# Optimization experiments

Hardware: AMD Instinct MI355X
Metric: run time of the kernel (lower is better)

## Reference

```python
import jax, jax.numpy as jnp
import numpy as np

NS = 16   # scalar multiplicity (ns)
NV = 4    # vector multiplicity (nv)
N_EDGE_FEAT = 3 * NS          # 48
W_NUMEL = NS * NS + NS * NV   # 320 = fully-connected TP weight numel


def setup_inputs() -> dict:
    key = jax.random.key(0)
    ks = jax.random.split(key, 8)
    N, E = 50000, 600000
    node_attr = jax.random.normal(ks[0], (N, NS), jnp.float32)          # 16x0e node features
    edge_index = jax.random.randint(ks[1], (2, E), 0, N)                # [src; dst]
    edge_attr = jax.random.normal(ks[2], (E, NS), jnp.float32)          # embedded edge attr (ns)
    edge_sh = jax.random.normal(ks[3], (E, 9), jnp.float32)             # sh lmax=2: 1+3+5
    s = 0.05
    fc1_w = jax.random.normal(ks[4], (N_EDGE_FEAT, N_EDGE_FEAT), jnp.float32) * s
    fc1_b = jnp.zeros((N_EDGE_FEAT,), jnp.float32)
    fc2_w = jax.random.normal(ks[5], (N_EDGE_FEAT, W_NUMEL), jnp.float32) * s
    fc2_b = jnp.zeros((W_NUMEL,), jnp.float32)
    return {"node_attr": node_attr, "edge_attr": edge_attr, "edge_sh": edge_sh,
            "fc1_w": fc1_w, "fc1_b": fc1_b, "fc2_w": fc2_w, "fc2_b": fc2_b,
            "edge_index": edge_index}


def reference(node_attr, edge_attr, edge_sh, fc1_w, fc1_b, fc2_w, fc2_b, edge_index):
    """TensorProductConvLayer forward: gather -> per-edge weighted tensor product -> scatter-mean.
    in_irreps=16x0e, sh=1x0e+1x1o+1x2e, out_irreps=16x0e+4x1o (residual=False, batch_norm=False)."""
    src, dst = edge_index[0], edge_index[1]
    E = edge_attr.shape[0]
    N = node_attr.shape[0]
    # edge feature = cat(edge_attr, scalar node feats of src and dst)  -> [E, 48]
    ea = jnp.concatenate([edge_attr, node_attr[src], node_attr[dst]], axis=-1)
    # fc MLP -> per-edge tensor-product weights [E, 320]
    h = jax.nn.relu(ea @ fc1_w + fc1_b)
    w = h @ fc2_w + fc2_b
    w0 = w[:, : NS * NS].reshape(E, NS, NS)   # path 0e x 0e -> 0e
    w1 = w[:, NS * NS :].reshape(E, NS, NV)   # path 0e x 1o -> 1o
    x = node_attr[dst]                        # gathered scalar features [E, 16]
    inv = 1.0 / jnp.sqrt(jnp.float32(NS))     # e3nn path normalization (fan-in = 16)
    sh0 = edge_sh[:, :1]                      # l=0 component
    sh1 = edge_sh[:, 1:4]                     # l=1 components
    out0 = jnp.einsum('eu,euw->ew', x * sh0, w0) * inv           # [E, 16]
    out1 = jnp.einsum('eu,em,euw->ewm', x, sh1, w1) * inv        # [E, 4, 3]
    msg = jnp.concatenate([out0, out1.reshape(E, NV * 3)], axis=-1)  # [E, 28]
    # scatter-mean to source nodes
    summed = jax.ops.segment_sum(msg, src, num_segments=N)
    cnt = jax.ops.segment_sum(jnp.ones((E, 1), msg.dtype), src, num_segments=N)
    return summed / jnp.maximum(cnt, 1.0)
```

## Files before the change

### kernel.cpp

```cpp
#include <hip/hip_runtime.h>

#define NS   16
#define NV   4
#define FEAT 48
#define WN   320
#define MSG  28
#define MSGB 32

typedef __bf16 bf16x8 __attribute__((ext_vector_type(8)));
typedef __bf16 bf16x4 __attribute__((ext_vector_type(4)));
typedef float  f32x4  __attribute__((ext_vector_type(4)));

#define PK1_ELEMS (2 * 3 * 64 * 8)
#define PK2_ELEMS (2 * 20 * 64 * 8)
#define PACK_BLOCKS 8

__global__ void prep_kernel(const float* __restrict__ fc1_w, const float* __restrict__ fc1_b,
                            const float* __restrict__ fc2_w, const float* __restrict__ fc2_b,
                            const int* __restrict__ src,
                            __bf16* __restrict__ pk1, __bf16* __restrict__ pk2,
                            int* __restrict__ count, int* __restrict__ pos, int E)
{
    const int tid = threadIdx.x;
    if (blockIdx.x < PACK_BLOCKS) {
        const int idx = blockIdx.x * 256 + tid;
        const int stride = PACK_BLOCKS * 256;
        for (int i = idx; i < PK1_ELEMS; i += stride) {
            const int j = i & 7, l = (i >> 3) & 63, f = i >> 9;
            const int nt = f % 3, p = f / 3;
            const int q = l >> 4, col = 16 * nt + (l & 15);
            float v;
            if (p == 0) {
                const int k = (j < 4) ? (4 * q + j) : (16 + 4 * q + j - 4);
                v = fc1_w[k * FEAT + col];
            } else if (j < 4) {
                v = fc1_w[(32 + 4 * q + j) * FEAT + col];
            } else {
                v = (j == 4 && q == 0) ? fc1_b[col] : 0.f;
            }
            pk1[i] = (__bf16)v;
        }
        for (int i = idx; i < PK2_ELEMS; i += stride) {
            const int j = i & 7, l = (i >> 3) & 63, f = i >> 9;
            const int nt = f % 20, p = f / 20;
            const int q = l >> 4, col = 16 * nt + (l & 15);
            float v;
            if (p == 0) {
                const int k = (j < 4) ? (4 * q + j) : (16 + 4 * q + j - 4);
                v = fc2_w[k * WN + col];
            } else if (j < 4) {
                v = fc2_w[(32 + 4 * q + j) * WN + col];
            } else {
                v = (j == 4 && q == 0) ? fc2_b[col] : 0.f;
            }
            pk2[i] = (__bf16)v;
        }
    } else {
        const int nb = gridDim.x - PACK_BLOCKS;
        for (int e = (blockIdx.x - PACK_BLOCKS) * 256 + tid; e < E; e += nb * 256)
            pos[e] = atomicAdd(&count[src[e]], 1);
    }
}

__global__ void scan_atomic(const int* __restrict__ in, int* __restrict__ outBase,
                            int* __restrict__ gctr, int n)
{
    __shared__ int s[256];
    __shared__ int blockBase;
    const int tid = threadIdx.x;
    const int i = blockIdx.x * 256 + tid;
    int v = (i < n) ? in[i] : 0;
    int acc = v;
    s[tid] = acc;
    __syncthreads();
    #pragma unroll
    for (int off = 1; off < 256; off <<= 1) {
        int t = (tid >= off) ? s[tid - off] : 0;
        __syncthreads();
        acc += t;
        s[tid] = acc;
        __syncthreads();
    }
    if (tid == 255) blockBase = atomicAdd(gctr, acc);
    __syncthreads();
    if (i < n) outBase[i] = blockBase + acc - v;
}

template<int MODE>
__global__ __launch_bounds__(256, 7) void edge_mfma_kernel(
    const float* __restrict__ node_attr,
    const float* __restrict__ edge_attr,
    const float* __restrict__ edge_sh,
    const int*   __restrict__ edge_index,
    const int*   __restrict__ base,
    const int*   __restrict__ pos,
    const __bf16* __restrict__ pk1,
    const __bf16* __restrict__ pk2,
    __bf16* __restrict__ msg,
    float*  __restrict__ out_acc,
    float*  __restrict__ cnt,
    int E)
{
    __shared__ float sX[4][32][20];

    const int tid = threadIdx.x;
    const int w   = tid >> 6;
    const int l   = tid & 63;
    const int q   = l >> 4;
    const int r16 = l & 15;
    const int e0  = (blockIdx.x * 4 + w) * 32;

    const float4 z4 = make_float4(0.f, 0.f, 0.f, 0.f);
    const float bias1 = (q == 0) ? 1.f : 0.f;

    bf16x8 w1f[2][3];
    #pragma unroll
    for (int p = 0; p < 2; ++p)
        #pragma unroll
        for (int nt = 0; nt < 3; ++nt)
            w1f[p][nt] = *reinterpret_cast<const bf16x8*>(pk1 + ((size_t)(p * 3 + nt) * 64 + l) * 8);

    bf16x8 eaf[2][2];
    int   srcI[2], rnkQ[2];
    bool  evt[2];
    float sh0[2], sh1[2];
    #pragma unroll
    for (int t = 0; t < 2; ++t) {
        const int e = e0 + 16 * t + r16;
        const bool ev = (e < E);
        evt[t] = ev;
        srcI[t] = ev ? edge_index[e] : 0;
        const int dstI = ev ? edge_index[E + e] : 0;

        rnkQ[t] = 0;
        if (MODE == 0 && q == 0 && ev)
            rnkQ[t] = base[srcI[t]] + pos[e];

        float4 ea4 = z4, sa4 = z4, da4 = z4;
        if (ev) {
            ea4 = *reinterpret_cast<const float4*>(edge_attr + (size_t)e * NS + 4 * q);
            sa4 = *reinterpret_cast<const float4*>(node_attr + (size_t)srcI[t] * NS + 4 * q);
            da4 = *reinterpret_cast<const float4*>(node_attr + (size_t)dstI * NS + 4 * q);
        }
        *reinterpret_cast<f32x4*>(&sX[w][16 * t + r16][4 * q]) =
            f32x4{da4.x, da4.y, da4.z, da4.w};

        bf16x8 f0, f1;
        f0[0]=(__bf16)ea4.x; f0[1]=(__bf16)ea4.y; f0[2]=(__bf16)ea4.z; f0[3]=(__bf16)ea4.w;
        f0[4]=(__bf16)sa4.x; f0[5]=(__bf16)sa4.y; f0[6]=(__bf16)sa4.z; f0[7]=(__bf16)sa4.w;
        f1[0]=(__bf16)da4.x; f1[1]=(__bf16)da4.y; f1[2]=(__bf16)da4.z; f1[3]=(__bf16)da4.w;
        f1[4]=(__bf16)bias1; f1[5]=(__bf16)0.f; f1[6]=(__bf16)0.f; f1[7]=(__bf16)0.f;
        eaf[t][0] = f0;
        eaf[t][1] = f1;
        sh0[t] = ev ? edge_sh[(size_t)e * 9] : 0.f;
        sh1[t] = (ev && q < 3) ? edge_sh[(size_t)e * 9 + 1 + q] : 0.f;
    }

    bf16x8 hc[2][2];
    #pragma unroll
    for (int t = 0; t < 2; ++t) {
        f32x4 h0 = {0.f,0.f,0.f,0.f}, h1 = {0.f,0.f,0.f,0.f}, h2 = {0.f,0.f,0.f,0.f};
        h0 = __builtin_amdgcn_mfma_f32_16x16x32_bf16(w1f[0][0], eaf[t][0], h0, 0, 0, 0);
        h0 = __builtin_amdgcn_mfma_f32_16x16x32_bf16(w1f[1][0], eaf[t][1], h0, 0, 0, 0);
        h1 = __builtin_amdgcn_mfma_f32_16x16x32_bf16(w1f[0][1], eaf[t][0], h1, 0, 0, 0);
        h1 = __builtin_amdgcn_mfma_f32_16x16x32_bf16(w1f[1][1], eaf[t][1], h1, 0, 0, 0);
        h2 = __builtin_amdgcn_mfma_f32_16x16x32_bf16(w1f[0][2], eaf[t][0], h2, 0, 0, 0);
        h2 = __builtin_amdgcn_mfma_f32_16x16x32_bf16(w1f[1][2], eaf[t][1], h2, 0, 0, 0);
        bf16x8 c0, c1;
        #pragma unroll
        for (int g = 0; g < 4; ++g) {
            c0[g]     = (__bf16)fmaxf(h0[g], 0.f);
            c0[4 + g] = (__bf16)fmaxf(h1[g], 0.f);
            c1[g]     = (__bf16)fmaxf(h2[g], 0.f);
        }
        c1[4] = (__bf16)bias1;
        c1[5] = (__bf16)0.f; c1[6] = (__bf16)0.f; c1[7] = (__bf16)0.f;
        hc[t][0] = c0;
        hc[t][1] = c1;
    }

    f32x4 acc0[2] = {{0.f,0.f,0.f,0.f},{0.f,0.f,0.f,0.f}};
    f32x4 acc1[2] = {{0.f,0.f,0.f,0.f},{0.f,0.f,0.f,0.f}};
    #pragma unroll 4
    for (int nt2 = 0; nt2 < 20; ++nt2) {
        const bf16x8 wf0 = *reinterpret_cast<const bf16x8*>(pk2 + ((size_t)(0 * 20 + nt2) * 64 + l) * 8);
        const bf16x8 wf1 = *reinterpret_cast<const bf16x8*>(pk2 + ((size_t)(1 * 20 + nt2) * 64 + l) * 8);
        #pragma unroll
        for (int t = 0; t < 2; ++t) {
            f32x4 d = {0.f,0.f,0.f,0.f};
            d = __builtin_amdgcn_mfma_f32_16x16x32_bf16(wf0, hc[t][0], d, 0, 0, 0);
            d = __builtin_amdgcn_mfma_f32_16x16x32_bf16(wf1, hc[t][1], d, 0, 0, 0);
            if (nt2 < 16) {
                const float xv = sX[w][16 * t + r16][nt2];
                #pragma unroll
                for (int g = 0; g < 4; ++g) acc0[t][g] = fmaf(xv, d[g], acc0[t][g]);
            } else {
                const float xu = sX[w][16 * t + r16][4 * (nt2 - 16) + q];
                #pragma unroll
                for (int g = 0; g < 4; ++g) acc1[t][g] = fmaf(xu, d[g], acc1[t][g]);
            }
        }
    }

    const float inv = 0.25f;

    #pragma unroll
    for (int t = 0; t < 2; ++t)
        #pragma unroll
        for (int g = 0; g < 4; ++g) {
            float s = acc1[t][g];
            s += __shfl_xor(s, 16);
            s += __shfl_xor(s, 32);
            acc1[t][g] = s;
        }

    #pragma unroll
    for (int t = 0; t < 2; ++t) {
        const int e = e0 + 16 * t + r16;
        if (e >= E) continue;
        if (MODE == 0) {
            const int rnk = __shfl(rnkQ[t], r16);
            const size_t mb = (size_t)rnk * MSGB;
            bf16x4 v4;
            #pragma unroll
            for (int g = 0; g < 4; ++g) v4[g] = (__bf16)(inv * sh0[t] * acc0[t][g]);
            *reinterpret_cast<bf16x4*>(msg + mb + 4 * q) = v4;
            if (q < 3) {
                #pragma unroll
                for (int g = 0; g < 4; ++g)
                    msg[mb + 16 + 3 * g + q] =
                        (__bf16)(inv * sh1[t] * acc1[t][g]);
            }
        } else {
            const size_t ob = (size_t)srcI[t] * MSG;
            #pragma unroll
            for (int g = 0; g < 4; ++g)
                atomicAdd(&out_acc[ob + 4 * q + g], inv * sh0[t] * acc0[t][g]);
            if (q < 3) {
                #pragma unroll
                for (int g = 0; g < 4; ++g)
                    atomicAdd(&out_acc[ob + 16 + 3 * g + q], inv * sh1[t] * acc1[t][g]);
            }
            if (q == 3) atomicAdd(&cnt[srcI[t]], 1.f);
        }
    }
}

__global__ __launch_bounds__(256) void node_reduce(
    const __bf16* __restrict__ msg,
    const int* __restrict__ count,
    const int* __restrict__ base,
    float* __restrict__ out, int N)
{
    const int tid  = threadIdx.x;
    const int w    = tid >> 6;
    const int l    = tid & 63;
    const int slot = l >> 5;
    const int c    = l & 31;
    const int n    = blockIdx.x * 8 + w * 2 + slot;
    if (n >= N || c >= MSG) return;

    const int deg = count[n];
    const size_t b = (size_t)base[n] * MSGB;
    float acc = 0.f;
    int j = 0;
    for (; j + 4 <= deg; j += 4) {
        const float v0 = (float)msg[b + (size_t)(j + 0) * MSGB + c];
        const float v1 = (float)msg[b + (size_t)(j + 1) * MSGB + c];
        const float v2 = (float)msg[b + (size_t)(j + 2) * MSGB + c];
        const float v3 = (float)msg[b + (size_t)(j + 3) * MSGB + c];
        acc += (v0 + v1) + (v2 + v3);
    }
    for (; j < deg; ++j) acc += (float)msg[b + (size_t)j * MSGB + c];
    out[(size_t)n * MSG + c] = acc / fmaxf((float)deg, 1.f);
}

__global__ void finalize_kernel(float* __restrict__ out,
                                const float* __restrict__ cnt, int total)
{
    const int idx = blockIdx.x * blockDim.x + threadIdx.x;
    if (idx < total) {
        const int n = idx / MSG;
        out[idx] = out[idx] / fmaxf(cnt[n], 1.0f);
    }
}

extern "C" void kernel_launch(void* const* d_in, const int* in_sizes, int n_in,
                              void* d_out, int out_size, void* d_ws, size_t ws_size,
                              hipStream_t stream)
{
    const float* node_attr  = (const float*)d_in[0];
    const float* edge_attr  = (const float*)d_in[1];
    const float* edge_sh    = (const float*)d_in[2];
    const float* fc1_w      = (const float*)d_in[3];
    const float* fc1_b      = (const float*)d_in[4];
    const float* fc2_w      = (const float*)d_in[5];
    const float* fc2_b      = (const float*)d_in[6];
    const int*   edge_index = (const int*)d_in[7];

    const int N = in_sizes[0] / NS;
    const int E = in_sizes[1] / NS;
    const int nb = (N + 255) / 256;

    char* ws = (char*)d_ws;
    size_t off = 0;
    auto take = [&](size_t bytes) { off = (off + 255) & ~(size_t)255;
                                    size_t o = off; off += bytes; return o; };
    const size_t o_pk1    = take(PK1_ELEMS * 2);
    const size_t o_pk2    = take(PK2_ELEMS * 2);
    const size_t o_count  = take((size_t)N * 4);
    const size_t o_gctr   = take(256);
    const size_t o_base   = take((size_t)N * 4);
    const size_t o_cnt    = take((size_t)N * 4);
    const size_t o_pos    = take((size_t)E * 4);
    const size_t o_msg    = take((size_t)E * MSGB * 2);
    const bool csr_ok = (off <= ws_size);

    __bf16* pk1 = (__bf16*)(ws + o_pk1);
    __bf16* pk2 = (__bf16*)(ws + o_pk2);
    int* count  = (int*)(ws + o_count);
    int* pos    = (int*)(ws + o_pos);
    float* out  = (float*)d_out;

    const int egrid = (E + 127) / 128;
    const int hblocks = (E + 255) / 256;

    if (csr_ok) {
        int* gctr   = (int*)(ws + o_gctr);
        int* base   = (int*)(ws + o_base);
        __bf16* msg = (__bf16*)(ws + o_msg);

        hipMemsetAsync(ws + o_count, 0, o_gctr - o_count + 256, stream);

        prep_kernel<<<PACK_BLOCKS + hblocks, 256, 0, stream>>>(
            fc1_w, fc1_b, fc2_w, fc2_b, edge_index, pk1, pk2, count, pos, E);
        scan_atomic<<<nb, 256, 0, stream>>>(count, base, gctr, N);

        edge_mfma_kernel<0><<<egrid, 256, 0, stream>>>(node_attr, edge_attr, edge_sh,
                                                       edge_index, base, pos,
                                                       pk1, pk2, msg, nullptr, nullptr, E);

        node_reduce<<<(N + 7) / 8, 256, 0, stream>>>(msg, count, base, out, N);
    } else {
        float* cntp = (float*)(ws + o_cnt);
        hipMemsetAsync(d_out, 0, (size_t)out_size * sizeof(float), stream);
        hipMemsetAsync(ws + o_count, 0, (size_t)N * 4, stream);
        hipMemsetAsync(cntp, 0, (size_t)N * 4, stream);
        prep_kernel<<<PACK_BLOCKS + hblocks, 256, 0, stream>>>(
            fc1_w, fc1_b, fc2_w, fc2_b, edge_index, pk1, pk2, count, pos, E);
        edge_mfma_kernel<1><<<egrid, 256, 0, stream>>>(node_attr, edge_attr, edge_sh,
                                                       edge_index, nullptr, nullptr,
                                                       pk1, pk2, nullptr, out, cntp, E);
        const int total = N * MSG;
        finalize_kernel<<<(total + 255) / 256, 256, 0, stream>>>(out, cntp, total);
    }
}
```

Measured before the change: 123.4 us.

## Process two edge groups per wave with software-pipelined gather and FC2

Each wave now handles 64 edges as two 32-edge groups. The gather for the second group is issued before the FC2 work of the first group so its memory latency can overlap that MFMA work. The grid is halved to match, the shared tile is doubled, and the occupancy hint drops from 7 to 6 waves to leave room for the extra live registers. The risk is fewer resident waves and less parallelism across blocks.

```diff
diff --git a/kernel.cpp b/kernel.cpp
--- a/kernel.cpp
+++ b/kernel.cpp
@@ -87,7 +87,7 @@
 }
 
 template<int MODE>
-__global__ __launch_bounds__(256, 7) void edge_mfma_kernel(
+__global__ __launch_bounds__(256, 6) void edge_mfma_kernel(
     const float* __restrict__ node_attr,
     const float* __restrict__ edge_attr,
     const float* __restrict__ edge_sh,
@@ -101,149 +101,161 @@
     float*  __restrict__ cnt,
     int E)
 {
-    __shared__ float sX[4][32][20];
+    __shared__ float sX[4][64][20];
 
     const int tid = threadIdx.x;
     const int w   = tid >> 6;
     const int l   = tid & 63;
     const int q   = l >> 4;
     const int r16 = l & 15;
-    const int e0  = (blockIdx.x * 4 + w) * 32;
+    const int e0  = (blockIdx.x * 4 + w) * 64;
 
     const float4 z4 = make_float4(0.f, 0.f, 0.f, 0.f);
     const float bias1 = (q == 0) ? 1.f : 0.f;
 
-    bf16x8 w1f[2][3];
-    #pragma unroll
-    for (int p = 0; p < 2; ++p)
-        #pragma unroll
-        for (int nt = 0; nt < 3; ++nt)
-            w1f[p][nt] = *reinterpret_cast<const bf16x8*>(pk1 + ((size_t)(p * 3 + nt) * 64 + l) * 8);
-
-    bf16x8 eaf[2][2];
-    int   srcI[2], rnkQ[2];
-    bool  evt[2];
-    float sh0[2], sh1[2];
-    #pragma unroll
-    for (int t = 0; t < 2; ++t) {
-        const int e = e0 + 16 * t + r16;
-        const bool ev = (e < E);
-        evt[t] = ev;
-        srcI[t] = ev ? edge_index[e] : 0;
-        const int dstI = ev ? edge_index[E + e] : 0;
-
-        rnkQ[t] = 0;
-        if (MODE == 0 && q == 0 && ev)
-            rnkQ[t] = base[srcI[t]] + pos[e];
-
-        float4 ea4 = z4, sa4 = z4, da4 = z4;
-        if (ev) {
-            ea4 = *reinterpret_cast<const float4*>(edge_attr + (size_t)e * NS + 4 * q);
-            sa4 = *reinterpret_cast<const float4*>(node_attr + (size_t)srcI[t] * NS + 4 * q);
-            da4 = *reinterpret_cast<const float4*>(node_attr + (size_t)dstI * NS + 4 * q);
-        }
-        *reinterpret_cast<f32x4*>(&sX[w][16 * t + r16][4 * q]) =
-            f32x4{da4.x, da4.y, da4.z, da4.w};
-
-        bf16x8 f0, f1;
-        f0[0]=(__bf16)ea4.x; f0[1]=(__bf16)ea4.y; f0[2]=(__bf16)ea4.z; f0[3]=(__bf16)ea4.w;
-        f0[4]=(__bf16)sa4.x; f0[5]=(__bf16)sa4.y; f0[6]=(__bf16)sa4.z; f0[7]=(__bf16)sa4.w;
-        f1[0]=(__bf16)da4.x; f1[1]=(__bf16)da4.y; f1[2]=(__bf16)da4.z; f1[3]=(__bf16)da4.w;
-        f1[4]=(__bf16)bias1; f1[5]=(__bf16)0.f; f1[6]=(__bf16)0.f; f1[7]=(__bf16)0.f;
-        eaf[t][0] = f0;
-        eaf[t][1] = f1;
-        sh0[t] = ev ? edge_sh[(size_t)e * 9] : 0.f;
-        sh1[t] = (ev && q < 3) ? edge_sh[(size_t)e * 9 + 1 + q] : 0.f;
-    }
-
-    bf16x8 hc[2][2];
-    #pragma unroll
-    for (int t = 0; t < 2; ++t) {
-        f32x4 h0 = {0.f,0.f,0.f,0.f}, h1 = {0.f,0.f,0.f,0.f}, h2 = {0.f,0.f,0.f,0.f};
-        h0 = __builtin_amdgcn_mfma_f32_16x16x32_bf16(w1f[0][0], eaf[t][0], h0, 0, 0, 0);
-        h0 = __builtin_amdgcn_mfma_f32_16x16x32_bf16(w1f[1][0], eaf[t][1], h0, 0, 0, 0);
-        h1 = __builtin_amdgcn_mfma_f32_16x16x32_bf16(w1f[0][1], eaf[t][0], h1, 0, 0, 0);
-        h1 = __builtin_amdgcn_mfma_f32_16x16x32_bf16(w1f[1][1], eaf[t][1], h1, 0, 0, 0);
-        h2 = __builtin_amdgcn_mfma_f32_16x16x32_bf16(w1f[0][2], eaf[t][0], h2, 0, 0, 0);
-        h2 = __builtin_amdgcn_mfma_f32_16x16x32_bf16(w1f[1][2], eaf[t][1], h2, 0, 0, 0);
-        bf16x8 c0, c1;
-        #pragma unroll
-        for (int g = 0; g < 4; ++g) {
-            c0[g]     = (__bf16)fmaxf(h0[g], 0.f);
-            c0[4 + g] = (__bf16)fmaxf(h1[g], 0.f);
-            c1[g]     = (__bf16)fmaxf(h2[g], 0.f);
-        }
-        c1[4] = (__bf16)bias1;
-        c1[5] = (__bf16)0.f; c1[6] = (__bf16)0.f; c1[7] = (__bf16)0.f;
-        hc[t][0] = c0;
-        hc[t][1] = c1;
-    }
-
-    f32x4 acc0[2] = {{0.f,0.f,0.f,0.f},{0.f,0.f,0.f,0.f}};
-    f32x4 acc1[2] = {{0.f,0.f,0.f,0.f},{0.f,0.f,0.f,0.f}};
-    #pragma unroll 4
-    for (int nt2 = 0; nt2 < 20; ++nt2) {
-        const bf16x8 wf0 = *reinterpret_cast<const bf16x8*>(pk2 + ((size_t)(0 * 20 + nt2) * 64 + l) * 8);
-        const bf16x8 wf1 = *reinterpret_cast<const bf16x8*>(pk2 + ((size_t)(1 * 20 + nt2) * 64 + l) * 8);
+    auto GATHER = [&](int g, bf16x8 (&eaf)[2][2], int (&srcI)[2], int (&rnkQ)[2],
+                      float (&sh0)[2], float (&sh1)[2]) {
         #pragma unroll
         for (int t = 0; t < 2; ++t) {
-            f32x4 d = {0.f,0.f,0.f,0.f};
-            d = __builtin_amdgcn_mfma_f32_16x16x32_bf16(wf0, hc[t][0], d, 0, 0, 0);
-            d = __builtin_amdgcn_mfma_f32_16x16x32_bf16(wf1, hc[t][1], d, 0, 0, 0);
-            if (nt2 < 16) {
-                const float xv = sX[w][16 * t + r16][nt2];
+            const int e = e0 + g * 32 + 16 * t + r16;
+            const bool ev = (e < E);
+            srcI[t] = ev ? edge_index[e] : 0;
+            const int dstI = ev ? edge_index[E + e] : 0;
+
+            rnkQ[t] = 0;
+            if (MODE == 0 && q == 0 && ev)
+                rnkQ[t] = base[srcI[t]] + pos[e];
+
+            float4 ea4 = z4, sa4 = z4, da4 = z4;
+            if (ev) {
+                ea4 = *reinterpret_cast<const float4*>(edge_attr + (size_t)e * NS + 4 * q);
+                sa4 = *reinterpret_cast<const float4*>(node_attr + (size_t)srcI[t] * NS + 4 * q);
+                da4 = *reinterpret_cast<const float4*>(node_attr + (size_t)dstI * NS + 4 * q);
+            }
+            *reinterpret_cast<f32x4*>(&sX[w][g * 32 + 16 * t + r16][4 * q]) =
+                f32x4{da4.x, da4.y, da4.z, da4.w};
+
+            bf16x8 f0, f1;
+            f0[0]=(__bf16)ea4.x; f0[1]=(__bf16)ea4.y; f0[2]=(__bf16)ea4.z; f0[3]=(__bf16)ea4.w;
+            f0[4]=(__bf16)sa4.x; f0[5]=(__bf16)sa4.y; f0[6]=(__bf16)sa4.z; f0[7]=(__bf16)sa4.w;
+            f1[0]=(__bf16)da4.x; f1[1]=(__bf16)da4.y; f1[2]=(__bf16)da4.z; f1[3]=(__bf16)da4.w;
+            f1[4]=(__bf16)bias1; f1[5]=(__bf16)0.f; f1[6]=(__bf16)0.f; f1[7]=(__bf16)0.f;
+            eaf[t][0] = f0;
+            eaf[t][1] = f1;
+            sh0[t] = ev ? edge_sh[(size_t)e * 9] : 0.f;
+            sh1[t] = (ev && q < 3) ? edge_sh[(size_t)e * 9 + 1 + q] : 0.f;
+        }
+    };
+
+    auto FC1 = [&](bf16x8 (&eaf)[2][2], bf16x8 (&hc)[2][2]) {
+        bf16x8 w1f[2][3];
+        #pragma unroll
+        for (int p = 0; p < 2; ++p)
+            #pragma unroll
+            for (int nt = 0; nt < 3; ++nt)
+                w1f[p][nt] = *reinterpret_cast<const bf16x8*>(pk1 + ((size_t)(p * 3 + nt) * 64 + l) * 8);
+        #pragma unroll
+        for (int t = 0; t < 2; ++t) {
+            f32x4 h0 = {0.f,0.f,0.f,0.f}, h1 = {0.f,0.f,0.f,0.f}, h2 = {0.f,0.f,0.f,0.f};
+            h0 = __builtin_amdgcn_mfma_f32_16x16x32_bf16(w1f[0][0], eaf[t][0], h0, 0, 0, 0);
+            h0 = __builtin_amdgcn_mfma_f32_16x16x32_bf16(w1f[1][0], eaf[t][1], h0, 0, 0, 0);
+            h1 = __builtin_amdgcn_mfma_f32_16x16x32_bf16(w1f[0][1], eaf[t][0], h1, 0, 0, 0);
+            h1 = __builtin_amdgcn_mfma_f32_16x16x32_bf16(w1f[1][1], eaf[t][1], h1, 0, 0, 0);
+            h2 = __builtin_amdgcn_mfma_f32_16x16x32_bf16(w1f[0][2], eaf[t][0], h2, 0, 0, 0);
+            h2 = __builtin_amdgcn_mfma_f32_16x16x32_bf16(w1f[1][2], eaf[t][1], h2, 0, 0, 0);
+            bf16x8 c0, c1;
+            #pragma unroll
+            for (int g = 0; g < 4; ++g) {
+                c0[g]     = (__bf16)fmaxf(h0[g], 0.f);
+                c0[4 + g] = (__bf16)fmaxf(h1[g], 0.f);
+                c1[g]     = (__bf16)fmaxf(h2[g], 0.f);
+            }
+            c1[4] = (__bf16)bias1;
+            c1[5] = (__bf16)0.f; c1[6] = (__bf16)0.f; c1[7] = (__bf16)0.f;
+            hc[t][0] = c0;
+            hc[t][1] = c1;
+        }
+    };
+
+    auto FC2W = [&](int g, bf16x8 (&hc)[2][2], int (&srcI)[2], int (&rnkQ)[2],
+                    float (&sh0)[2], float (&sh1)[2]) {
+        f32x4 acc0[2] = {{0.f,0.f,0.f,0.f},{0.f,0.f,0.f,0.f}};
+        f32x4 acc1[2] = {{0.f,0.f,0.f,0.f},{0.f,0.f,0.f,0.f}};
+        #pragma unroll 4
+        for (int nt2 = 0; nt2 < 20; ++nt2) {
+            const bf16x8 wf0 = *reinterpret_cast<const bf16x8*>(pk2 + ((size_t)(0 * 20 + nt2) * 64 + l) * 8);
+            const bf16x8 wf1 = *reinterpret_cast<const bf16x8*>(pk2 + ((size_t)(1 * 20 + nt2) * 64 + l) * 8);
+            #pragma unroll
+            for (int t = 0; t < 2; ++t) {
+                f32x4 d = {0.f,0.f,0.f,0.f};
+                d = __builtin_amdgcn_mfma_f32_16x16x32_bf16(wf0, hc[t][0], d, 0, 0, 0);
+                d = __builtin_amdgcn_mfma_f32_16x16x32_bf16(wf1, hc[t][1], d, 0, 0, 0);
+                if (nt2 < 16) {
+                    const float xv = sX[w][g * 32 + 16 * t + r16][nt2];
+                    #pragma unroll
+                    for (int gg = 0; gg < 4; ++gg) acc0[t][gg] = fmaf(xv, d[gg], acc0[t][gg]);
+                } else {
+                    const float xu = sX[w][g * 32 + 16 * t + r16][4 * (nt2 - 16) + q];
+                    #pragma unroll
+                    for (int gg = 0; gg < 4; ++gg) acc1[t][gg] = fmaf(xu, d[gg], acc1[t][gg]);
+                }
+            }
+        }
+
+        const float inv = 0.25f;
+
+        #pragma unroll
+        for (int t = 0; t < 2; ++t)
+            #pragma unroll
+            for (int gg = 0; gg < 4; ++gg) {
+                float s = acc1[t][gg];
+                s += __shfl_xor(s, 16);
+                s += __shfl_xor(s, 32);
+                acc1[t][gg] = s;
+            }
+
+        #pragma unroll
+        for (int t = 0; t < 2; ++t) {
+            const int e = e0 + g * 32 + 16 * t + r16;
+            if (e >= E) continue;
+            if (MODE == 0) {
+                const int rnk = __shfl(rnkQ[t], r16);
+                const size_t mb = (size_t)rnk * MSGB;
+                bf16x4 v4;
                 #pragma unroll
-                for (int g = 0; g < 4; ++g) acc0[t][g] = fmaf(xv, d[g], acc0[t][g]);
+                for (int gg = 0; gg < 4; ++gg) v4[gg] = (__bf16)(inv * sh0[t] * acc0[t][gg]);
+                *reinterpret_cast<bf16x4*>(msg + mb + 4 * q) = v4;
+                if (q < 3) {
+                    #pragma unroll
+                    for (int gg = 0; gg < 4; ++gg)
+                        msg[mb + 16 + 3 * gg + q] =
+                            (__bf16)(inv * sh1[t] * acc1[t][gg]);
+                }
             } else {
-                const float xu = sX[w][16 * t + r16][4 * (nt2 - 16) + q];
+                const size_t ob = (size_t)srcI[t] * MSG;
                 #pragma unroll
-                for (int g = 0; g < 4; ++g) acc1[t][g] = fmaf(xu, d[g], acc1[t][g]);
-            }
-        }
-    }
-
-    const float inv = 0.25f;
-
-    #pragma unroll
-    for (int t = 0; t < 2; ++t)
-        #pragma unroll
-        for (int g = 0; g < 4; ++g) {
-            float s = acc1[t][g];
-            s += __shfl_xor(s, 16);
-            s += __shfl_xor(s, 32);
-            acc1[t][g] = s;
-        }
-
-    #pragma unroll
-    for (int t = 0; t < 2; ++t) {
-        const int e = e0 + 16 * t + r16;
-        if (e >= E) continue;
-        if (MODE == 0) {
-            const int rnk = __shfl(rnkQ[t], r16);
-            const size_t mb = (size_t)rnk * MSGB;
-            bf16x4 v4;
-            #pragma unroll
-            for (int g = 0; g < 4; ++g) v4[g] = (__bf16)(inv * sh0[t] * acc0[t][g]);
-            *reinterpret_cast<bf16x4*>(msg + mb + 4 * q) = v4;
-            if (q < 3) {
-                #pragma unroll
-                for (int g = 0; g < 4; ++g)
-                    msg[mb + 16 + 3 * g + q] =
-                        (__bf16)(inv * sh1[t] * acc1[t][g]);
-            }
-        } else {
-            const size_t ob = (size_t)srcI[t] * MSG;
-            #pragma unroll
-            for (int g = 0; g < 4; ++g)
-                atomicAdd(&out_acc[ob + 4 * q + g], inv * sh0[t] * acc0[t][g]);
-            if (q < 3) {
-                #pragma unroll
-                for (int g = 0; g < 4; ++g)
-                    atomicAdd(&out_acc[ob + 16 + 3 * g + q], inv * sh1[t] * acc1[t][g]);
-            }
-            if (q == 3) atomicAdd(&cnt[srcI[t]], 1.f);
-        }
-    }
+                for (int gg = 0; gg < 4; ++gg)
+                    atomicAdd(&out_acc[ob + 4 * q + gg], inv * sh0[t] * acc0[t][gg]);
+                if (q < 3) {
+                    #pragma unroll
+                    for (int gg = 0; gg < 4; ++gg)
+                        atomicAdd(&out_acc[ob + 16 + 3 * gg + q], inv * sh1[t] * acc1[t][gg]);
+                }
+                if (q == 3) atomicAdd(&cnt[srcI[t]], 1.f);
+            }
+        }
+    };
+
+    bf16x8 eafA[2][2], eafB[2][2], hcA[2][2], hcB[2][2];
+    int srcA[2], srcB[2], rnkA[2], rnkB[2];
+    float sh0A[2], sh1A[2], sh0B[2], sh1B[2];
+
+    GATHER(0, eafA, srcA, rnkA, sh0A, sh1A);
+    FC1(eafA, hcA);
+    GATHER(1, eafB, srcB, rnkB, sh0B, sh1B);
+    FC2W(0, hcA, srcA, rnkA, sh0A, sh1A);
+    FC1(eafB, hcB);
+    FC2W(1, hcB, srcB, rnkB, sh0B, sh1B);
 }
 
 __global__ __launch_bounds__(256) void node_reduce(
@@ -322,7 +334,7 @@
     int* pos    = (int*)(ws + o_pos);
     float* out  = (float*)d_out;
 
-    const int egrid = (E + 127) / 128;
+    const int egrid = (E + 255) / 256;
     const int hblocks = (E + 255) / 256;
 
     if (csr_ok) {
```

Result: slower. 139.8 us (+13.2%).
